# Kernel optimization log

Hardware: AMD Instinct MI355X
Metric: run time of the kernel (lower is better)

Reference implementation:

```python
import jax, jax.numpy as jnp
import numpy as np

E = 100000   # n_entities
R = 64       # n_relations
I = 256      # in_channels
O = 256      # out_channels
N_EDGES = 1_600_000


def setup_inputs() -> dict:
    key = jax.random.key(0)
    k1, k2, k3, k4 = jax.random.split(key, 4)
    x = jax.random.normal(k1, (E, I), dtype=jnp.float32)
    # cs must be nonzero (it is reciprocated); uniform in [0.5, 1.5)
    cs = jax.random.uniform(k2, (E, R), dtype=jnp.float32) + 0.5
    W = jax.random.normal(k3, (R, I, O), dtype=jnp.float32) * 0.05
    edge_index = jax.random.randint(k4, (2, N_EDGES), 0, E, dtype=jnp.int64)
    return {"x": x, "cs": cs, "W": W, "edge_index": edge_index}


def reference(x, cs, W, edge_index):
    # Faithful to: torch.einsum('er,rio,ej->eo', 1/cs, W, x)
    # i and j are independently contracted indices, so this factorizes:
    # out[e,o] = (sum_j x[e,j]) * sum_r (1/cs[e,r]) * (sum_i W[r,i,o])
    cs_reciprocal = 1.0 / cs                 # (E, R)
    W_sum = jnp.sum(W, axis=1)               # (R, O)
    x_sum = jnp.sum(x, axis=1)               # (E,)
    src = (cs_reciprocal @ W_sum) * x_sum[:, None]  # (E, O)
    return src
```

## Files before the change

### kernel.cpp

```cpp
#include <hip/hip_runtime.h>


constexpr int En = 100000;
constexpr int Rn = 64;
constexpr int In = 256;
constexpr int On = 256;
constexpr int TILES = En / 16;

typedef short bf16x8 __attribute__((ext_vector_type(8)));
typedef float floatx4 __attribute__((ext_vector_type(4)));

static __device__ __forceinline__ short f2bf(float f) {
    unsigned u = __builtin_bit_cast(unsigned, f);
    unsigned r = (u + 0x7FFFu + ((u >> 16) & 1u)) >> 16;
    return (short)r;
}

__global__ __launch_bounds__(1024) void wsum_kernel(const float* __restrict__ W,
                                                    short* __restrict__ wsumT) {
    __shared__ float red[16][65];
    const int r  = blockIdx.x >> 2;
    const int h  = blockIdx.x & 3;
    const int ol = threadIdx.x & 63;
    const int ic = threadIdx.x >> 6;
    const int o  = h * 64 + ol;
    const float* base = W + ((size_t)r * In + (size_t)ic * 16) * On + o;
    float s = 0.f;
#pragma unroll
    for (int i = 0; i < 16; ++i) s += base[(size_t)i * On];
    red[ic][ol] = s;
    __syncthreads();
    if (ic == 0) {
        float t = 0.f;
#pragma unroll
        for (int j = 0; j < 16; ++j) t += red[j][ol];
        wsumT[o * Rn + r] = f2bf(t);
    }
}

__global__ __launch_bounds__(256) void xsum_kernel(const float* __restrict__ x,
                                                   float* __restrict__ xsum,
                                                   int xstride) {
    const int w    = (blockIdx.x * 256 + (int)threadIdx.x) >> 6;
    const int nw   = (gridDim.x * 256) >> 6;
    const int lane = threadIdx.x & 63;
    for (int base = w * 4; base < En; base += nw * 4) {
        float s[4];
#pragma unroll
        for (int u = 0; u < 4; ++u) {
            const int row = base + u;
            float4 v = make_float4(0.f, 0.f, 0.f, 0.f);
            if (row < En)
                v = *(const float4*)&x[(size_t)row * In + lane * 4];
            s[u] = (v.x + v.y) + (v.z + v.w);
        }
#pragma unroll
        for (int u = 0; u < 4; ++u) {
#pragma unroll
            for (int off = 32; off; off >>= 1) s[u] += __shfl_down(s[u], off, 64);
        }
        if (lane == 0) {
#pragma unroll
            for (int u = 0; u < 4; ++u)
                if (base + u < En) xsum[(size_t)(base + u) * xstride] = s[u];
        }
    }
}

__global__ __launch_bounds__(256) void out_kernel(const float* __restrict__ cs,
                                                  const short* __restrict__ wsumT,
                                                  const float* __restrict__ xsum,
                                                  int xstride,
                                                  float* __restrict__ out) {
    const int gw = (blockIdx.x * 256 + (int)threadIdx.x) >> 6;
    const int nw = (gridDim.x * 256) >> 6;
    const int ln = threadIdx.x & 63;
    const int lm = ln & 15;
    const int q  = ln >> 4;

    bf16x8 wa0[16], wa1[16];
#pragma unroll
    for (int ot = 0; ot < 16; ++ot) {
        const short* p = wsumT + ((ot * 16 + lm) * Rn + q * 8);
        wa0[ot] = *(const bf16x8*)p;
        wa1[ot] = *(const bf16x8*)(p + 32);
    }

    int t = gw;
    if (t >= TILES) return;
    float4 c0, c1, c2, c3;
    float xv;
    {
        const float* p = cs + (size_t)(t * 16 + lm) * Rn + q * 8;
        c0 = *(const float4*)p;        c1 = *(const float4*)(p + 4);
        c2 = *(const float4*)(p + 32); c3 = *(const float4*)(p + 36);
        xv = xsum[(size_t)(t * 16 + lm) * xstride];
    }
    while (true) {
        const int tn = t + nw;
        const float4 d0 = c0, d1 = c1, d2 = c2, d3 = c3;
        const float xs = xv;
        if (tn < TILES) {
            const float* p = cs + (size_t)(tn * 16 + lm) * Rn + q * 8;
            c0 = *(const float4*)p;        c1 = *(const float4*)(p + 4);
            c2 = *(const float4*)(p + 32); c3 = *(const float4*)(p + 36);
            xv = xsum[(size_t)(tn * 16 + lm) * xstride];
        }
        bf16x8 b0, b1;
        {
            const float rv[16] = {d0.x, d0.y, d0.z, d0.w, d1.x, d1.y, d1.z, d1.w,
                                  d2.x, d2.y, d2.z, d2.w, d3.x, d3.y, d3.z, d3.w};
#pragma unroll
            for (int j = 0; j < 8; ++j) {
                b0[j] = f2bf(__builtin_amdgcn_rcpf(rv[j]));
                b1[j] = f2bf(__builtin_amdgcn_rcpf(rv[8 + j]));
            }
        }
        float* orow = out + (size_t)(t * 16 + lm) * On + q * 4;
#pragma unroll
        for (int ot = 0; ot < 16; ++ot) {
            floatx4 acc = {0.f, 0.f, 0.f, 0.f};
            acc = __builtin_amdgcn_mfma_f32_16x16x32_bf16(wa0[ot], b0, acc, 0, 0, 0);
            acc = __builtin_amdgcn_mfma_f32_16x16x32_bf16(wa1[ot], b1, acc, 0, 0, 0);
            const float4 st = make_float4(acc[0] * xs, acc[1] * xs,
                                          acc[2] * xs, acc[3] * xs);
            *(float4*)(orow + ot * 16) = st;
        }
        if (tn >= TILES) break;
        t = tn;
    }
}

extern "C" void kernel_launch(void* const* d_in, const int* in_sizes, int n_in,
                              void* d_out, int out_size, void* d_ws, size_t ws_size,
                              hipStream_t stream) {
    const float* x  = (const float*)d_in[0];
    const float* cs = (const float*)d_in[1];
    const float* W  = (const float*)d_in[2];
    float* out = (float*)d_out;

    short* wsumT = (short*)d_ws;
    float* xsum;
    int xstride;
    if (ws_size >= (size_t)(32768 + En * 4)) {
        xsum = (float*)((char*)d_ws + 32768);
        xstride = 1;
    } else {
        xsum = out;
        xstride = On;
    }

    wsum_kernel<<<dim3(256), dim3(1024), 0, stream>>>(W, wsumT);
    xsum_kernel<<<dim3(2048), dim3(256), 0, stream>>>(x, xsum, xstride);
    out_kernel<<<dim3(512), dim3(256), 0, stream>>>(cs, wsumT, xsum, xstride, out);
}
```

Measured before the change: 232.1 us.

## Merge W and x reductions into one kernel; one tile per wave in output kernel

Merges the W-sum and x-sum reduction kernels into a single launch whose blocks branch on block index, removing one kernel launch and letting both reductions run concurrently. The output kernel drops its persistent grid-stride loop with register-cached W fragments and software prefetch. Instead it launches one wave per 16-row tile and reloads the small bf16 W-sum fragments from cache on each iteration, with launch bounds raised for occupancy. This trades explicit prefetching and register reuse for more waves in flight, and adds repeated loads of the W-sum table.

After: 243.3 us. +4.8%, slower.

```diff
diff --git a/kernel.cpp b/kernel.cpp
--- a/kernel.cpp
+++ b/kernel.cpp
@@ -6,6 +6,9 @@
 constexpr int In = 256;
 constexpr int On = 256;
 constexpr int TILES = En / 16;
+
+constexpr int WSUM_BLOCKS = 256;
+constexpr int XSUM_BLOCKS = 512;
 
 typedef short bf16x8 __attribute__((ext_vector_type(8)));
 typedef float floatx4 __attribute__((ext_vector_type(4)));
@@ -16,118 +19,101 @@
     return (short)r;
 }
 
-__global__ __launch_bounds__(1024) void wsum_kernel(const float* __restrict__ W,
-                                                    short* __restrict__ wsumT) {
-    __shared__ float red[16][65];
-    const int r  = blockIdx.x >> 2;
-    const int h  = blockIdx.x & 3;
-    const int ol = threadIdx.x & 63;
-    const int ic = threadIdx.x >> 6;
-    const int o  = h * 64 + ol;
-    const float* base = W + ((size_t)r * In + (size_t)ic * 16) * On + o;
-    float s = 0.f;
-#pragma unroll
-    for (int i = 0; i < 16; ++i) s += base[(size_t)i * On];
-    red[ic][ol] = s;
-    __syncthreads();
-    if (ic == 0) {
-        float t = 0.f;
-#pragma unroll
-        for (int j = 0; j < 16; ++j) t += red[j][ol];
-        wsumT[o * Rn + r] = f2bf(t);
-    }
-}
-
-__global__ __launch_bounds__(256) void xsum_kernel(const float* __restrict__ x,
+__global__ __launch_bounds__(1024) void pre_kernel(const float* __restrict__ W,
+                                                   const float* __restrict__ x,
+                                                   short* __restrict__ wsumT,
                                                    float* __restrict__ xsum,
                                                    int xstride) {
-    const int w    = (blockIdx.x * 256 + (int)threadIdx.x) >> 6;
-    const int nw   = (gridDim.x * 256) >> 6;
-    const int lane = threadIdx.x & 63;
-    for (int base = w * 4; base < En; base += nw * 4) {
-        float s[4];
+    __shared__ float red[16][65];
+    if (blockIdx.x < WSUM_BLOCKS) {
+        const int r  = blockIdx.x >> 2;
+        const int h  = blockIdx.x & 3;
+        const int ol = threadIdx.x & 63;
+        const int ic = threadIdx.x >> 6;
+        const int o  = h * 64 + ol;
+        const float* base = W + ((size_t)r * In + (size_t)ic * 16) * On + o;
+        float s = 0.f;
 #pragma unroll
-        for (int u = 0; u < 4; ++u) {
-            const int row = base + u;
-            float4 v = make_float4(0.f, 0.f, 0.f, 0.f);
-            if (row < En)
-                v = *(const float4*)&x[(size_t)row * In + lane * 4];
-            s[u] = (v.x + v.y) + (v.z + v.w);
+        for (int i = 0; i < 16; ++i) s += base[(size_t)i * On];
+        red[ic][ol] = s;
+        __syncthreads();
+        if (ic == 0) {
+            float t = 0.f;
+#pragma unroll
+            for (int j = 0; j < 16; ++j) t += red[j][ol];
+            wsumT[o * Rn + r] = f2bf(t);
         }
+    } else {
+        const int w    = ((int)(blockIdx.x - WSUM_BLOCKS) * 1024 + (int)threadIdx.x) >> 6;
+        const int nw   = (XSUM_BLOCKS * 1024) >> 6;
+        const int lane = threadIdx.x & 63;
+        for (int base = w * 4; base < En; base += nw * 4) {
+            float s[4];
 #pragma unroll
-        for (int u = 0; u < 4; ++u) {
+            for (int u = 0; u < 4; ++u) {
+                const int row = base + u;
+                float4 v = make_float4(0.f, 0.f, 0.f, 0.f);
+                if (row < En)
+                    v = *(const float4*)&x[(size_t)row * In + lane * 4];
+                s[u] = (v.x + v.y) + (v.z + v.w);
+            }
 #pragma unroll
-            for (int off = 32; off; off >>= 1) s[u] += __shfl_down(s[u], off, 64);
-        }
-        if (lane == 0) {
+            for (int u = 0; u < 4; ++u) {
 #pragma unroll
-            for (int u = 0; u < 4; ++u)
-                if (base + u < En) xsum[(size_t)(base + u) * xstride] = s[u];
+                for (int off = 32; off; off >>= 1) s[u] += __shfl_down(s[u], off, 64);
+            }
+            if (lane == 0) {
+#pragma unroll
+                for (int u = 0; u < 4; ++u)
+                    if (base + u < En) xsum[(size_t)(base + u) * xstride] = s[u];
+            }
         }
     }
 }
 
-__global__ __launch_bounds__(256) void out_kernel(const float* __restrict__ cs,
-                                                  const short* __restrict__ wsumT,
-                                                  const float* __restrict__ xsum,
-                                                  int xstride,
-                                                  float* __restrict__ out) {
+__global__ __launch_bounds__(256, 4) void out_kernel(const float* __restrict__ cs,
+                                                     const short* __restrict__ wsumT,
+                                                     const float* __restrict__ xsum,
+                                                     int xstride,
+                                                     float* __restrict__ out) {
     const int gw = (blockIdx.x * 256 + (int)threadIdx.x) >> 6;
-    const int nw = (gridDim.x * 256) >> 6;
+    if (gw >= TILES) return;
     const int ln = threadIdx.x & 63;
     const int lm = ln & 15;
     const int q  = ln >> 4;
+    const int e0 = gw * 16 + lm;
 
-    bf16x8 wa0[16], wa1[16];
+    const float* p = cs + (size_t)e0 * Rn + q * 8;
+    const float4 d0 = *(const float4*)p;
+    const float4 d1 = *(const float4*)(p + 4);
+    const float4 d2 = *(const float4*)(p + 32);
+    const float4 d3 = *(const float4*)(p + 36);
+    const float xs  = xsum[(size_t)e0 * xstride];
+
+    bf16x8 b0, b1;
+    {
+        const float rv[16] = {d0.x, d0.y, d0.z, d0.w, d1.x, d1.y, d1.z, d1.w,
+                              d2.x, d2.y, d2.z, d2.w, d3.x, d3.y, d3.z, d3.w};
+#pragma unroll
+        for (int j = 0; j < 8; ++j) {
+            b0[j] = f2bf(__builtin_amdgcn_rcpf(rv[j]));
+            b1[j] = f2bf(__builtin_amdgcn_rcpf(rv[8 + j]));
+        }
+    }
+
+    float* orow = out + (size_t)e0 * On + q * 4;
+    const short* wb = wsumT + lm * Rn + q * 8;
 #pragma unroll
     for (int ot = 0; ot < 16; ++ot) {
-        const short* p = wsumT + ((ot * 16 + lm) * Rn + q * 8);
-        wa0[ot] = *(const bf16x8*)p;
-        wa1[ot] = *(const bf16x8*)(p + 32);
-    }
-
-    int t = gw;
-    if (t >= TILES) return;
-    float4 c0, c1, c2, c3;
-    float xv;
-    {
-        const float* p = cs + (size_t)(t * 16 + lm) * Rn + q * 8;
-        c0 = *(const float4*)p;        c1 = *(const float4*)(p + 4);
-        c2 = *(const float4*)(p + 32); c3 = *(const float4*)(p + 36);
-        xv = xsum[(size_t)(t * 16 + lm) * xstride];
-    }
-    while (true) {
-        const int tn = t + nw;
-        const float4 d0 = c0, d1 = c1, d2 = c2, d3 = c3;
-        const float xs = xv;
-        if (tn < TILES) {
-            const float* p = cs + (size_t)(tn * 16 + lm) * Rn + q * 8;
-            c0 = *(const float4*)p;        c1 = *(const float4*)(p + 4);
-            c2 = *(const float4*)(p + 32); c3 = *(const float4*)(p + 36);
-            xv = xsum[(size_t)(tn * 16 + lm) * xstride];
-        }
-        bf16x8 b0, b1;
-        {
-            const float rv[16] = {d0.x, d0.y, d0.z, d0.w, d1.x, d1.y, d1.z, d1.w,
-                                  d2.x, d2.y, d2.z, d2.w, d3.x, d3.y, d3.z, d3.w};
-#pragma unroll
-            for (int j = 0; j < 8; ++j) {
-                b0[j] = f2bf(__builtin_amdgcn_rcpf(rv[j]));
-                b1[j] = f2bf(__builtin_amdgcn_rcpf(rv[8 + j]));
-            }
-        }
-        float* orow = out + (size_t)(t * 16 + lm) * On + q * 4;
-#pragma unroll
-        for (int ot = 0; ot < 16; ++ot) {
-            floatx4 acc = {0.f, 0.f, 0.f, 0.f};
-            acc = __builtin_amdgcn_mfma_f32_16x16x32_bf16(wa0[ot], b0, acc, 0, 0, 0);
-            acc = __builtin_amdgcn_mfma_f32_16x16x32_bf16(wa1[ot], b1, acc, 0, 0, 0);
-            const float4 st = make_float4(acc[0] * xs, acc[1] * xs,
-                                          acc[2] * xs, acc[3] * xs);
-            *(float4*)(orow + ot * 16) = st;
-        }
-        if (tn >= TILES) break;
-        t = tn;
+        const short* wp = wb + ot * 16 * Rn;
+        const bf16x8 wa0 = *(const bf16x8*)wp;
+        const bf16x8 wa1 = *(const bf16x8*)(wp + 32);
+        floatx4 acc = {0.f, 0.f, 0.f, 0.f};
+        acc = __builtin_amdgcn_mfma_f32_16x16x32_bf16(wa0, b0, acc, 0, 0, 0);
+        acc = __builtin_amdgcn_mfma_f32_16x16x32_bf16(wa1, b1, acc, 0, 0, 0);
+        const float4 st = make_float4(acc[0] * xs, acc[1] * xs,
+                                      acc[2] * xs, acc[3] * xs);
+        *(float4*)(orow + ot * 16) = st;
     }
 }
 
@@ -150,7 +136,8 @@
         xstride = On;
     }
 
-    wsum_kernel<<<dim3(256), dim3(1024), 0, stream>>>(W, wsumT);
-    xsum_kernel<<<dim3(2048), dim3(256), 0, stream>>>(x, xsum, xstride);
-    out_kernel<<<dim3(512), dim3(256), 0, stream>>>(cs, wsumT, xsum, xstride, out);
+    pre_kernel<<<dim3(WSUM_BLOCKS + XSUM_BLOCKS), dim3(1024), 0, stream>>>(
+        W, x, wsumT, xsum, xstride);
+    out_kernel<<<dim3((TILES * 64 + 255) / 256), dim3(256), 0, stream>>>(
+        cs, wsumT, xsum, xstride, out);
 }
```
